# Optimization experiments

Hardware: AMD Instinct MI355X
Metric: run time of the kernel (lower is better)

Reference implementation:

```python
import jax, jax.numpy as jnp
import numpy as np

HEAD = 16
DIM = 1024
HEAD_DIM = DIM // HEAD


def setup_inputs() -> dict:
    key = jax.random.key(0)
    k1, k2, k3, k4 = jax.random.split(key, 4)
    x = jax.random.normal(k1, (2, 2048, DIM), dtype=jnp.float32)
    # nn.Linear(dim, 3*dim, bias=False): weight [3*dim, dim]
    w_qkv = jax.random.normal(k2, (3 * DIM, DIM), dtype=jnp.float32) * (DIM ** -0.5)
    # output proj nn.Linear(dim, dim)
    w_out = jax.random.normal(k3, (DIM, DIM), dtype=jnp.float32) * (DIM ** -0.5)
    b_out = jax.random.normal(k4, (DIM,), dtype=jnp.float32) * 0.01
    return {"x": x, "w_qkv": w_qkv, "w_out": w_out, "b_out": b_out}


def reference(x, w_qkv, w_out, b_out):
    b, s, _ = x.shape
    scale = HEAD_DIM ** -0.5
    qkv = jnp.einsum('bsd,ed->bse', x, w_qkv)  # [b, s, 3*dim]
    q, k, v = jnp.split(qkv, 3, axis=-1)
    def split_heads(t):
        return t.reshape(b, s, HEAD, HEAD_DIM).transpose(0, 2, 1, 3)  # b h s d
    q, k, v = split_heads(q), split_heads(k), split_heads(v)
    scores = jnp.einsum('bhqd,bhkd->bhqk', q, k) * scale
    attn = jax.nn.softmax(scores, axis=-1)
    out = jnp.einsum('bhqk,bhkd->bhqd', attn, v)
    out = out.transpose(0, 2, 1, 3).reshape(b, s, DIM)
    out = jnp.einsum('bsd,ed->bse', out, w_out) + b_out
    return out
```

## Files before the change

### kernel.cpp

```cpp
#include <hip/hip_runtime.h>
#include <hip/hip_bf16.h>
#include <stdint.h>

typedef __bf16 bf16_t;
typedef __attribute__((ext_vector_type(8))) __bf16 bf16x8;
typedef __attribute__((ext_vector_type(4))) __bf16 bf16x4v;
typedef __attribute__((ext_vector_type(4))) float f32x4;

#define GLOBAL_AS __attribute__((address_space(1)))
#define LDS_AS __attribute__((address_space(3)))

__device__ __forceinline__ void gload_lds16(const bf16_t* g, bf16_t* l) {
  __builtin_amdgcn_global_load_lds((const GLOBAL_AS void*)g, (LDS_AS void*)l, 16, 0, 0);
}

__global__ void cvt_f32_bf16(const float* __restrict__ in, bf16_t* __restrict__ out, int n) {
  int i = (blockIdx.x * 256 + threadIdx.x) * 4;
  if (i + 3 < n) {
    float4 v = *(const float4*)(in + i);
    bf16x4v o;
    o[0] = (bf16_t)v.x; o[1] = (bf16_t)v.y; o[2] = (bf16_t)v.z; o[3] = (bf16_t)v.w;
    *(bf16x4v*)(out + i) = o;
  }
}

template<int EPI>
__global__ __launch_bounds__(256)
void gemm_tn(const bf16_t* __restrict__ A, const bf16_t* __restrict__ B,
             void* __restrict__ Cout, const float* __restrict__ bias,
             int K, int ldc, int qcols, float qscale)
{
  __shared__ __align__(16) bf16_t As[128 * 32];
  __shared__ __align__(16) bf16_t Bs[128 * 32];
  const int t  = threadIdx.x;
  const int l  = t & 63, w = t >> 6;
  const int wm = w >> 1, wn = w & 1;
  const int lo = l & 15, hi = l >> 4;
  const int brow = blockIdx.y * 128;
  const int bcol = blockIdx.x * 128;

  const int i0 = t, i1 = t + 256;
  const int r0 = i0 >> 2, c0 = i0 & 3;
  const int r1 = i1 >> 2, c1 = i1 & 3;

  f32x4 acc[4][4] = {};

  for (int k0 = 0; k0 < K; k0 += 32) {
    gload_lds16(A + (size_t)(brow + r0) * K + k0 + c0 * 8, As + i0 * 8);
    gload_lds16(A + (size_t)(brow + r1) * K + k0 + c1 * 8, As + i1 * 8);
    gload_lds16(B + (size_t)(bcol + r0) * K + k0 + c0 * 8, Bs + i0 * 8);
    gload_lds16(B + (size_t)(bcol + r1) * K + k0 + c1 * 8, Bs + i1 * 8);
    __syncthreads();

    bf16x8 a[4], bb[4];
#pragma unroll
    for (int fm = 0; fm < 4; fm++)
      a[fm] = *(const bf16x8*)(As + (wm * 64 + fm * 16 + lo) * 32 + hi * 8);
#pragma unroll
    for (int fn = 0; fn < 4; fn++)
      bb[fn] = *(const bf16x8*)(Bs + (wn * 64 + fn * 16 + lo) * 32 + hi * 8);

#pragma unroll
    for (int fm = 0; fm < 4; fm++)
#pragma unroll
      for (int fn = 0; fn < 4; fn++)
        acc[fm][fn] = __builtin_amdgcn_mfma_f32_16x16x32_bf16(a[fm], bb[fn], acc[fm][fn], 0, 0, 0);
    __syncthreads();
  }

#pragma unroll
  for (int fm = 0; fm < 4; fm++) {
#pragma unroll
    for (int fn = 0; fn < 4; fn++) {
#pragma unroll
      for (int j = 0; j < 4; j++) {
        int row = brow + wm * 64 + fm * 16 + hi * 4 + j;
        int col = bcol + wn * 64 + fn * 16 + lo;
        float v = acc[fm][fn][j];
        if (EPI == 0) {
          if (col < qcols) v *= qscale;
          ((bf16_t*)Cout)[(size_t)row * ldc + col] = (bf16_t)v;
        } else {
          ((float*)Cout)[(size_t)row * ldc + col] = v + bias[col];
        }
      }
    }
  }
}

#define LDK 72

__global__ __launch_bounds__(512, 2)
void flash_attn(const bf16_t* __restrict__ qkv, bf16_t* __restrict__ aout)
{
  __shared__ __align__(16) bf16_t Kl[64 * LDK];
  __shared__ __align__(16) bf16_t Vt[64 * LDK];
  __shared__ __align__(16) bf16_t Pl[8][32 * LDK];

  const int t = threadIdx.x;
  const int l = t & 63, w = t >> 6;
  const int lo = l & 15, hi = l >> 4;
  int bid = (int)blockIdx.x;
  bid = (bid & 7) * 32 + (bid >> 3);
  const int qblk = bid & 7;
  const int bh   = bid >> 3;
  const int b = bh >> 4, h = bh & 15;
  const int rowbase = b * 2048;
  const int q0 = qblk * 256 + w * 32;

  const int r = l & 7, c = l >> 3;
  const int krow0 = w * 8 + r;
  const bf16_t* kp = qkv + (size_t)(rowbase + krow0) * 3072 + h * 64 + c * 8 + 1024;
  const bf16_t* vp = kp + 1024;
  const size_t step = (size_t)64 * 3072;

  bf16x8 aq[2][2];
#pragma unroll
  for (int fm = 0; fm < 2; fm++)
#pragma unroll
    for (int kb = 0; kb < 2; kb++)
      aq[fm][kb] = *(const bf16x8*)(qkv + (size_t)(rowbase + q0 + fm * 16 + lo) * 3072
                                    + h * 64 + kb * 32 + hi * 8);

  bf16x8 ones;
#pragma unroll
  for (int j = 0; j < 8; j++) ones[j] = (bf16_t)1.0f;

  f32x4 oacc[2][4] = {};
  f32x4 ssum[2] = {};

  bf16x8 kch = *(const bf16x8*)kp;
  bf16x8 vch = *(const bf16x8*)vp;

  bf16_t* plw = &Pl[w][0];

  for (int it = 0; it < 32; ++it) {
    __syncthreads();
    *(bf16x8*)(Kl + krow0 * LDK + c * 8) = kch;
    {
      union { bf16x8 v; uint32_t u[4]; } tv; tv.v = vch;
      uint32_t a0 = __shfl_xor((int)tv.u[2], 4, 64);
      uint32_t a1 = __shfl_xor((int)tv.u[3], 4, 64);
      uint32_t a2 = __shfl_xor((int)tv.u[0], 4, 64);
      uint32_t a3 = __shfl_xor((int)tv.u[1], 4, 64);
      bool s4 = (l & 4) != 0;
      uint32_t n0 = s4 ? a0 : tv.u[0];
      uint32_t n1 = s4 ? a1 : tv.u[1];
      uint32_t n2 = s4 ? tv.u[2] : a2;
      uint32_t n3 = s4 ? tv.u[3] : a3;
      uint32_t b0 = __shfl_xor((int)n1, 2, 64);
      uint32_t b1 = __shfl_xor((int)n0, 2, 64);
      uint32_t b2 = __shfl_xor((int)n3, 2, 64);
      uint32_t b3 = __shfl_xor((int)n2, 2, 64);
      bool s2 = (l & 2) != 0;
      uint32_t m0 = s2 ? b0 : n0;
      uint32_t m1 = s2 ? n1 : b1;
      uint32_t m2 = s2 ? b2 : n2;
      uint32_t m3 = s2 ? n3 : b3;
      uint32_t c0 = __shfl_xor((int)m0, 1, 64);
      uint32_t c1 = __shfl_xor((int)m1, 1, 64);
      uint32_t c2 = __shfl_xor((int)m2, 1, 64);
      uint32_t c3 = __shfl_xor((int)m3, 1, 64);
      bool odd = (l & 1) != 0;
      union { uint32_t u[4]; bf16x8 v; } tw;
      tw.u[0] = odd ? ((m0 & 0xFFFF0000u) | (c0 >> 16)) : ((m0 & 0xFFFFu) | (c0 << 16));
      tw.u[1] = odd ? ((m1 & 0xFFFF0000u) | (c1 >> 16)) : ((m1 & 0xFFFFu) | (c1 << 16));
      tw.u[2] = odd ? ((m2 & 0xFFFF0000u) | (c2 >> 16)) : ((m2 & 0xFFFFu) | (c2 << 16));
      tw.u[3] = odd ? ((m3 & 0xFFFF0000u) | (c3 >> 16)) : ((m3 & 0xFFFFu) | (c3 << 16));
      *(bf16x8*)(Vt + (c * 8 + r) * LDK + w * 8) = tw.v;
    }
    __syncthreads();

    if (it < 31) {
      kp += step; vp += step;
      kch = *(const bf16x8*)kp;
      vch = *(const bf16x8*)vp;
    }

    bf16x8 kf[4][2];
#pragma unroll
    for (int fn = 0; fn < 4; fn++)
#pragma unroll
      for (int kb = 0; kb < 2; kb++)
        kf[fn][kb] = *(const bf16x8*)(Kl + (fn * 16 + lo) * LDK + kb * 32 + hi * 8);
    f32x4 sacc[2][4] = {};
#pragma unroll
    for (int fm = 0; fm < 2; fm++)
#pragma unroll
      for (int fn = 0; fn < 4; fn++)
#pragma unroll
        for (int kb = 0; kb < 2; kb++)
          sacc[fm][fn] = __builtin_amdgcn_mfma_f32_16x16x32_bf16(aq[fm][kb], kf[fn][kb], sacc[fm][fn], 0, 0, 0);

#pragma unroll
    for (int fm = 0; fm < 2; fm++)
#pragma unroll
      for (int fn = 0; fn < 4; fn++)
#pragma unroll
        for (int j = 0; j < 4; j++)
          plw[(fm * 16 + hi * 4 + j) * LDK + fn * 16 + lo] =
              (bf16_t)__builtin_amdgcn_exp2f(sacc[fm][fn][j]);
    asm volatile("s_waitcnt lgkmcnt(0)" ::: "memory");
    __builtin_amdgcn_sched_barrier(0);

    bf16x8 pa[2][2], vb[4][2];
#pragma unroll
    for (int fm = 0; fm < 2; fm++)
#pragma unroll
      for (int kb = 0; kb < 2; kb++)
        pa[fm][kb] = *(const bf16x8*)(plw + (fm * 16 + lo) * LDK + kb * 32 + hi * 8);
#pragma unroll
    for (int fd = 0; fd < 4; fd++)
#pragma unroll
      for (int kb = 0; kb < 2; kb++)
        vb[fd][kb] = *(const bf16x8*)(Vt + (fd * 16 + lo) * LDK + kb * 32 + hi * 8);
#pragma unroll
    for (int fm = 0; fm < 2; fm++)
#pragma unroll
      for (int kb = 0; kb < 2; kb++)
        ssum[fm] = __builtin_amdgcn_mfma_f32_16x16x32_bf16(pa[fm][kb], ones, ssum[fm], 0, 0, 0);
#pragma unroll
    for (int fm = 0; fm < 2; fm++)
#pragma unroll
      for (int fd = 0; fd < 4; fd++)
#pragma unroll
        for (int kb = 0; kb < 2; kb++)
          oacc[fm][fd] = __builtin_amdgcn_mfma_f32_16x16x32_bf16(pa[fm][kb], vb[fd][kb], oacc[fm][fd], 0, 0, 0);
  }

#pragma unroll
  for (int fm = 0; fm < 2; fm++)
#pragma unroll
    for (int j = 0; j < 4; j++) {
      float inv = 1.0f / ssum[fm][j];
      int row = rowbase + q0 + fm * 16 + hi * 4 + j;
#pragma unroll
      for (int fd = 0; fd < 4; fd++) {
        int col = h * 64 + fd * 16 + lo;
        aout[(size_t)row * 1024 + col] = (bf16_t)(oacc[fm][fd][j] * inv);
      }
    }
}

extern "C" void kernel_launch(void* const* d_in, const int* in_sizes, int n_in,
                              void* d_out, int out_size, void* d_ws, size_t ws_size,
                              hipStream_t stream) {
  const float* x     = (const float*)d_in[0];
  const float* w_qkv = (const float*)d_in[1];
  const float* w_out = (const float*)d_in[2];
  const float* b_out = (const float*)d_in[3];

  char* ws = (char*)d_ws;
  bf16_t* xb   = (bf16_t*)(ws);
  bf16_t* wqb  = (bf16_t*)(ws + 8388608);
  bf16_t* wob  = (bf16_t*)(ws + 14680064);
  bf16_t* qkvb = (bf16_t*)(ws + 16777216);
  bf16_t* aob  = (bf16_t*)(ws + 41943040);

  cvt_f32_bf16<<<4096, 256, 0, stream>>>(x,     xb,  4194304);
  cvt_f32_bf16<<<3072, 256, 0, stream>>>(w_qkv, wqb, 3145728);
  cvt_f32_bf16<<<1024, 256, 0, stream>>>(w_out, wob, 1048576);

  dim3 g1(24, 32);
  gemm_tn<0><<<g1, 256, 0, stream>>>(xb, wqb, qkvb, nullptr, 1024, 3072, 1024, 0.18033688011f);

  flash_attn<<<256, 512, 0, stream>>>(qkvb, aob);

  dim3 g2(8, 32);
  gemm_tn<1><<<g2, 256, 0, stream>>>(aob, wob, d_out, b_out, 1024, 1024, 0, 1.0f);
}
```

Measured before the change: 141.5 us.

## Halve attention block size, double grid, and pack P stores with permuted key layout

The attention kernel now runs 512 blocks of 4 waves (128 query rows each) instead of 256 blocks of 8 waves, and each thread stages two K rows and two V chunks per iteration. The softmax P tile is written as packed 4-element bf16 stores in a permuted key order, and the V rows each thread loads are permuted to match, so the PV product stays consistent. The aim is better occupancy and CU balance across the 256 CUs, plus fewer, wider LDS stores. In exchange each block loads K/V for fewer queries, which doubles total K/V global traffic.

```diff
diff --git a/kernel.cpp b/kernel.cpp
--- a/kernel.cpp
+++ b/kernel.cpp
@@ -12,6 +12,45 @@
 
 __device__ __forceinline__ void gload_lds16(const bf16_t* g, bf16_t* l) {
   __builtin_amdgcn_global_load_lds((const GLOBAL_AS void*)g, (LDS_AS void*)l, 16, 0, 0);
+}
+
+__device__ __forceinline__ uint32_t pk2(float a, float b) {
+  union { bf16_t h[2]; uint32_t u; } x;
+  x.h[0] = (bf16_t)a; x.h[1] = (bf16_t)b;
+  return x.u;
+}
+
+__device__ __forceinline__ bf16x8 xpose8(bf16x8 v, int l) {
+  union { bf16x8 v; uint32_t u[4]; } tv; tv.v = v;
+  uint32_t a0 = __shfl_xor((int)tv.u[2], 4, 64);
+  uint32_t a1 = __shfl_xor((int)tv.u[3], 4, 64);
+  uint32_t a2 = __shfl_xor((int)tv.u[0], 4, 64);
+  uint32_t a3 = __shfl_xor((int)tv.u[1], 4, 64);
+  bool s4 = (l & 4) != 0;
+  uint32_t n0 = s4 ? a0 : tv.u[0];
+  uint32_t n1 = s4 ? a1 : tv.u[1];
+  uint32_t n2 = s4 ? tv.u[2] : a2;
+  uint32_t n3 = s4 ? tv.u[3] : a3;
+  uint32_t b0 = __shfl_xor((int)n1, 2, 64);
+  uint32_t b1 = __shfl_xor((int)n0, 2, 64);
+  uint32_t b2 = __shfl_xor((int)n3, 2, 64);
+  uint32_t b3 = __shfl_xor((int)n2, 2, 64);
+  bool s2 = (l & 2) != 0;
+  uint32_t m0 = s2 ? b0 : n0;
+  uint32_t m1 = s2 ? n1 : b1;
+  uint32_t m2 = s2 ? b2 : n2;
+  uint32_t m3 = s2 ? n3 : b3;
+  uint32_t c0 = __shfl_xor((int)m0, 1, 64);
+  uint32_t c1 = __shfl_xor((int)m1, 1, 64);
+  uint32_t c2 = __shfl_xor((int)m2, 1, 64);
+  uint32_t c3 = __shfl_xor((int)m3, 1, 64);
+  bool odd = (l & 1) != 0;
+  union { uint32_t u[4]; bf16x8 v; } tw;
+  tw.u[0] = odd ? ((m0 & 0xFFFF0000u) | (c0 >> 16)) : ((m0 & 0xFFFFu) | (c0 << 16));
+  tw.u[1] = odd ? ((m1 & 0xFFFF0000u) | (c1 >> 16)) : ((m1 & 0xFFFFu) | (c1 << 16));
+  tw.u[2] = odd ? ((m2 & 0xFFFF0000u) | (c2 >> 16)) : ((m2 & 0xFFFFu) | (c2 << 16));
+  tw.u[3] = odd ? ((m3 & 0xFFFF0000u) | (c3 >> 16)) : ((m3 & 0xFFFFu) | (c3 << 16));
+  return tw.v;
 }
 
 __global__ void cvt_f32_bf16(const float* __restrict__ in, bf16_t* __restrict__ out, int n) {
@@ -90,28 +129,28 @@
 
 #define LDK 72
 
-__global__ __launch_bounds__(512, 2)
+__global__ __launch_bounds__(256, 2)
 void flash_attn(const bf16_t* __restrict__ qkv, bf16_t* __restrict__ aout)
 {
   __shared__ __align__(16) bf16_t Kl[64 * LDK];
   __shared__ __align__(16) bf16_t Vt[64 * LDK];
-  __shared__ __align__(16) bf16_t Pl[8][32 * LDK];
+  __shared__ __align__(16) bf16_t Pl[4][32 * LDK];
 
   const int t = threadIdx.x;
   const int l = t & 63, w = t >> 6;
   const int lo = l & 15, hi = l >> 4;
   int bid = (int)blockIdx.x;
-  bid = (bid & 7) * 32 + (bid >> 3);
-  const int qblk = bid & 7;
-  const int bh   = bid >> 3;
+  bid = (bid & 7) * 64 + (bid >> 3);
+  const int qblk = bid & 15;
+  const int bh   = bid >> 4;
   const int b = bh >> 4, h = bh & 15;
   const int rowbase = b * 2048;
-  const int q0 = qblk * 256 + w * 32;
+  const int q0 = qblk * 128 + w * 32;
 
   const int r = l & 7, c = l >> 3;
-  const int krow0 = w * 8 + r;
-  const bf16_t* kp = qkv + (size_t)(rowbase + krow0) * 3072 + h * 64 + c * 8 + 1024;
-  const bf16_t* vp = kp + 1024;
+  const int krow_w = w * 16 + r;
+  const int vkey_w = 4 * w + (r >> 2) + 16 * (r & 3);
+  const bf16_t* kvbase = qkv + (size_t)rowbase * 3072 + h * 64 + 1024;
   const size_t step = (size_t)64 * 3072;
 
   bf16x8 aq[2][2];
@@ -129,52 +168,33 @@
   f32x4 oacc[2][4] = {};
   f32x4 ssum[2] = {};
 
-  bf16x8 kch = *(const bf16x8*)kp;
-  bf16x8 vch = *(const bf16x8*)vp;
+  bf16x8 kch[2], vch[2];
+#pragma unroll
+  for (int i = 0; i < 2; i++) {
+    kch[i] = *(const bf16x8*)(kvbase + (size_t)(krow_w + i * 8) * 3072 + c * 8);
+    vch[i] = *(const bf16x8*)(kvbase + 1024 + (size_t)(vkey_w + 2 * i) * 3072 + c * 8);
+  }
 
   bf16_t* plw = &Pl[w][0];
+  const bf16_t* kv_next = kvbase + step;
 
   for (int it = 0; it < 32; ++it) {
     __syncthreads();
-    *(bf16x8*)(Kl + krow0 * LDK + c * 8) = kch;
-    {
-      union { bf16x8 v; uint32_t u[4]; } tv; tv.v = vch;
-      uint32_t a0 = __shfl_xor((int)tv.u[2], 4, 64);
-      uint32_t a1 = __shfl_xor((int)tv.u[3], 4, 64);
-      uint32_t a2 = __shfl_xor((int)tv.u[0], 4, 64);
-      uint32_t a3 = __shfl_xor((int)tv.u[1], 4, 64);
-      bool s4 = (l & 4) != 0;
-      uint32_t n0 = s4 ? a0 : tv.u[0];
-      uint32_t n1 = s4 ? a1 : tv.u[1];
-      uint32_t n2 = s4 ? tv.u[2] : a2;
-      uint32_t n3 = s4 ? tv.u[3] : a3;
-      uint32_t b0 = __shfl_xor((int)n1, 2, 64);
-      uint32_t b1 = __shfl_xor((int)n0, 2, 64);
-      uint32_t b2 = __shfl_xor((int)n3, 2, 64);
-      uint32_t b3 = __shfl_xor((int)n2, 2, 64);
-      bool s2 = (l & 2) != 0;
-      uint32_t m0 = s2 ? b0 : n0;
-      uint32_t m1 = s2 ? n1 : b1;
-      uint32_t m2 = s2 ? b2 : n2;
-      uint32_t m3 = s2 ? n3 : b3;
-      uint32_t c0 = __shfl_xor((int)m0, 1, 64);
-      uint32_t c1 = __shfl_xor((int)m1, 1, 64);
-      uint32_t c2 = __shfl_xor((int)m2, 1, 64);
-      uint32_t c3 = __shfl_xor((int)m3, 1, 64);
-      bool odd = (l & 1) != 0;
-      union { uint32_t u[4]; bf16x8 v; } tw;
-      tw.u[0] = odd ? ((m0 & 0xFFFF0000u) | (c0 >> 16)) : ((m0 & 0xFFFFu) | (c0 << 16));
-      tw.u[1] = odd ? ((m1 & 0xFFFF0000u) | (c1 >> 16)) : ((m1 & 0xFFFFu) | (c1 << 16));
-      tw.u[2] = odd ? ((m2 & 0xFFFF0000u) | (c2 >> 16)) : ((m2 & 0xFFFFu) | (c2 << 16));
-      tw.u[3] = odd ? ((m3 & 0xFFFF0000u) | (c3 >> 16)) : ((m3 & 0xFFFFu) | (c3 << 16));
-      *(bf16x8*)(Vt + (c * 8 + r) * LDK + w * 8) = tw.v;
+#pragma unroll
+    for (int i = 0; i < 2; i++) {
+      *(bf16x8*)(Kl + (krow_w + i * 8) * LDK + c * 8) = kch[i];
+      bf16x8 tw = xpose8(vch[i], l);
+      *(bf16x8*)(Vt + (c * 8 + r) * LDK + (w * 2 + i) * 8) = tw;
     }
     __syncthreads();
 
     if (it < 31) {
-      kp += step; vp += step;
-      kch = *(const bf16x8*)kp;
-      vch = *(const bf16x8*)vp;
+#pragma unroll
+      for (int i = 0; i < 2; i++) {
+        kch[i] = *(const bf16x8*)(kv_next + (size_t)(krow_w + i * 8) * 3072 + c * 8);
+        vch[i] = *(const bf16x8*)(kv_next + 1024 + (size_t)(vkey_w + 2 * i) * 3072 + c * 8);
+      }
+      kv_next += step;
     }
 
     bf16x8 kf[4][2];
@@ -195,11 +215,15 @@
 #pragma unroll
     for (int fm = 0; fm < 2; fm++)
 #pragma unroll
-      for (int fn = 0; fn < 4; fn++)
-#pragma unroll
-        for (int j = 0; j < 4; j++)
-          plw[(fm * 16 + hi * 4 + j) * LDK + fn * 16 + lo] =
-              (bf16_t)__builtin_amdgcn_exp2f(sacc[fm][fn][j]);
+      for (int j = 0; j < 4; j++) {
+        float p0 = __builtin_amdgcn_exp2f(sacc[fm][0][j]);
+        float p1 = __builtin_amdgcn_exp2f(sacc[fm][1][j]);
+        float p2 = __builtin_amdgcn_exp2f(sacc[fm][2][j]);
+        float p3 = __builtin_amdgcn_exp2f(sacc[fm][3][j]);
+        int row = fm * 16 + hi * 4 + j;
+        uint2 d2; d2.x = pk2(p0, p1); d2.y = pk2(p2, p3);
+        *(uint2*)(plw + row * LDK + lo * 4) = d2;
+      }
     asm volatile("s_waitcnt lgkmcnt(0)" ::: "memory");
     __builtin_amdgcn_sched_barrier(0);
 
@@ -264,7 +288,7 @@
   dim3 g1(24, 32);
   gemm_tn<0><<<g1, 256, 0, stream>>>(xb, wqb, qkvb, nullptr, 1024, 3072, 1024, 0.18033688011f);
 
-  flash_attn<<<256, 512, 0, stream>>>(qkvb, aob);
+  flash_attn<<<512, 256, 0, stream>>>(qkvb, aob);
 
   dim3 g2(8, 32);
   gemm_tn<1><<<g2, 256, 0, stream>>>(aob, wob, d_out, b_out, 1024, 1024, 0, 1.0f);
```

Result: slower. 146.8 us (+3.7%).
